# Kernel tuning notes

Hardware: AMD Instinct MI355X
Metric: run time of the kernel (lower is better)

The kernel has to match this reference:

```python
import jax, jax.numpy as jnp
import numpy as np

B = 512            # number of graphs in the batch
P = 256            # nodes per graph (== max_graph_size, graphs are equal-sized)
N = B * P          # total nodes
E = 2 * 1024 * 1024
F = 64             # node_feat_size
LAYERS = [32, 32, 32, 1]


def setup_inputs() -> dict:
    key = jax.random.key(0)
    ks = jax.random.split(key, 16)
    x = jax.random.normal(ks[0], (N, F), dtype=jnp.float32)
    edge_index = jax.random.randint(ks[1], (2, E), 0, N, dtype=jnp.int32)
    batch = (jnp.arange(N, dtype=jnp.int32) // P)   # sorted graph ids, equal sizes
    edge_mask = jax.random.uniform(ks[2], (E,), dtype=jnp.float32)
    # layer weights (DGCNN layer: out = D^-1 @ A_tilde @ X @ W + b)
    dims = [F] + LAYERS
    params = {}
    for i in range(len(LAYERS)):
        fan = dims[i]
        params[f"W{i}"] = jax.random.normal(ks[3 + 2 * i], (dims[i], dims[i + 1]), dtype=jnp.float32) / np.sqrt(fan)
        params[f"b{i}"] = jnp.zeros((dims[i + 1],), dtype=jnp.float32)
    return {"x": x, "edge_index": edge_index, "batch": batch, "edge_mask": edge_mask, **params}


def _build_matrices(x, edge_index, batch, edge_mask):
    # counts / exclusive starts per graph (batch is sorted)
    ones = jnp.ones_like(batch)
    counts = jax.ops.segment_sum(ones, batch, num_segments=B)
    starts = jnp.cumsum(counts) - counts                       # [B]
    src, dst = edge_index[0], edge_index[1]
    g = batch[src]
    valid = (batch[src] == batch[dst])                          # drop cross-graph edges
    ls = jnp.clip(src - starts[g], 0, P - 1)
    ld = jnp.clip(dst - starts[g], 0, P - 1)
    w = jnp.where(valid, edge_mask, 0.0)
    # padded A_tilde = A + I  (duplicate edges accumulate, as sparse COO add does)
    adj = jnp.zeros((B, P, P), dtype=x.dtype).at[g, ls, ld].add(w)
    adj = adj + jnp.eye(P, dtype=x.dtype)[None]
    # reciprocal degree of A_tilde, nan/inf -> 0
    deg = adj.sum(axis=2)                                       # [B, P]
    rinv = jnp.where(deg > 0, 1.0 / deg, 0.0)
    feats = x.reshape(B, P, F)                                  # equal-size graphs -> trivial pad
    return adj, rinv, feats


def reference(x, edge_index, batch, edge_mask, W0, b0, W1, b1, W2, b2, W3, b3):
    adj, rinv, h = _build_matrices(x, edge_index, batch, edge_mask)
    for W, b in ((W0, b0), (W1, b1), (W2, b2), (W3, b3)):
        h = jnp.einsum('bnm,bmf->bnf', adj, h @ W)              # A_tilde @ X @ W
        h = rinv[..., None] * h + b                             # D^-1 scaling + bias
        h = jnp.tanh(h)
    return h
```

## Files before the change

kernel.cpp:

```cpp
#include <hip/hip_runtime.h>
#include <hip/hip_bf16.h>

#define BGR 512
#define PP  256
#define NN  (BGR * PP)
#define EE  (2 * 1024 * 1024)
#define RCAP 4


__global__ void k_escatter(const int* __restrict__ ei, const float* __restrict__ emask,
                           int* __restrict__ rowcnt, int2* __restrict__ ebkt) {
    int e0 = (blockIdx.x * 256 + threadIdx.x) * 4;
    int4 s4 = *reinterpret_cast<const int4*>(ei + e0);
    int4 d4 = *reinterpret_cast<const int4*>(ei + EE + e0);
#pragma unroll
    for (int j = 0; j < 4; j++) {
        int s = (&s4.x)[j];
        int d = (&d4.x)[j];
        if ((s >> 8) != (d >> 8)) continue;
        float w = emask[e0 + j];
        int pos = atomicAdd(&rowcnt[s], 1);
        if (pos < RCAP) ebkt[s * RCAP + pos] = make_int2(d & 255, __float_as_int(w));
    }
}

__device__ __forceinline__ float fast_tanh(float x) {
    float t = __expf(2.0f * x);
    return 1.0f - __fdividef(2.0f, 1.0f + t);
}

template <int KH>
__device__ __forceinline__ void pmv32(const float (&h)[KH], const float* __restrict__ W,
                                      float (&P)[32]) {
#pragma unroll
    for (int c = 0; c < 32; c++) P[c] = 0.f;
#pragma unroll
    for (int k = 0; k < KH; k++) {
        const float hk = h[k];
#pragma unroll
        for (int c = 0; c < 32; c++) P[c] += hk * W[k * 32 + c];
    }
}

__global__ __launch_bounds__(512, 4)
void k_fused(const float* __restrict__ x,
             const float* __restrict__ W0, const float* __restrict__ b0,
             const float* __restrict__ W1, const float* __restrict__ b1,
             const float* __restrict__ W2, const float* __restrict__ b2,
             const float* __restrict__ W3, const float* __restrict__ b3,
             const int* __restrict__ rowcnt, const int2* __restrict__ ebkt,
             float* __restrict__ out) {
    __shared__ float Psl[2][PP][36];

    const int t    = threadIdx.x;
    const int g    = blockIdx.x;
    const int row  = t & 255;
    const int half = __builtin_amdgcn_readfirstlane(t >> 8);
    const int cb   = half * 16;

    const int node = g * PP + row;

    const int cnt = min(rowcnt[node], RCAP);
    int   eld[RCAP];
    float ewt[RCAP];
    float wsum = 0.f;
#pragma unroll
    for (int j = 0; j < RCAP; j++) {
        if (j < cnt) {
            int2 v = ebkt[node * RCAP + j];
            eld[j] = v.x;
            ewt[j] = __int_as_float(v.y);
            wsum += ewt[j];
        } else {
            eld[j] = row;
            ewt[j] = 0.f;
        }
    }
    const float rv = 1.0f / (1.0f + wsum);

    float xr[32];
    const float* xrow = x + (size_t)node * 64 + half * 32;
#pragma unroll
    for (int k = 0; k < 32; k += 4) {
        float4 v = *reinterpret_cast<const float4*>(xrow + k);
        xr[k] = v.x; xr[k + 1] = v.y; xr[k + 2] = v.z; xr[k + 3] = v.w;
    }

    float P[32];
    float acc[16];
    float h[16];

    const float* Ws0 = W0 + half * (32 * 32);
    const float* Ws1 = W1 + half * (16 * 32);
    const float* Ws2 = W2 + half * (16 * 32);

    float (*own)[36]       = Psl[half];
    const float (*par)[36] = Psl[1 - half];
    const float (*sA)[36]  = Psl[0];
    const float (*sB)[36]  = Psl[1];

#pragma unroll
    for (int L = 0; L < 3; L++) {
        if (L == 0)      pmv32<32>(xr, Ws0, P);
        else if (L == 1) pmv32<16>(h, Ws1, P);
        else             pmv32<16>(h, Ws2, P);

#pragma unroll
        for (int j = 0; j < 32; j += 4)
            *reinterpret_cast<float4*>(&own[row][j]) =
                make_float4(P[j], P[j + 1], P[j + 2], P[j + 3]);
        __syncthreads();

#pragma unroll
        for (int j = 0; j < 16; j += 4) {
            float4 q = *reinterpret_cast<const float4*>(&par[row][cb + j]);
            acc[j]     = P[cb + j]     + q.x;
            acc[j + 1] = P[cb + j + 1] + q.y;
            acc[j + 2] = P[cb + j + 2] + q.z;
            acc[j + 3] = P[cb + j + 3] + q.w;
        }

#pragma unroll
        for (int e = 0; e < RCAP; e++) {
            if (ewt[e] != 0.f) {
                int ld = eld[e];
                float w = ewt[e];
#pragma unroll
                for (int j = 0; j < 16; j += 4) {
                    float4 ya = *reinterpret_cast<const float4*>(&sA[ld][cb + j]);
                    float4 yb = *reinterpret_cast<const float4*>(&sB[ld][cb + j]);
                    acc[j]     += w * (ya.x + yb.x);
                    acc[j + 1] += w * (ya.y + yb.y);
                    acc[j + 2] += w * (ya.z + yb.z);
                    acc[j + 3] += w * (ya.w + yb.w);
                }
            }
        }

        const float* b = (L == 0) ? b0 : (L == 1) ? b1 : b2;
#pragma unroll
        for (int j = 0; j < 16; j++) h[j] = fast_tanh(rv * acc[j] + b[cb + j]);
        __syncthreads();
    }

    float a = 0.f;
#pragma unroll
    for (int k = 0; k < 16; k++) a += h[k] * W3[cb + k];
    Psl[0][row][32 + half] = a;
    __syncthreads();
    if (half == 0) {
        float z = Psl[0][row][32] + Psl[0][row][33];
#pragma unroll
        for (int e = 0; e < RCAP; e++) {
            if (ewt[e] != 0.f) {
                int ld = eld[e];
                z += ewt[e] * (Psl[0][ld][32] + Psl[0][ld][33]);
            }
        }
        out[node] = fast_tanh(rv * z + b3[0]);
    }
}


extern "C" void kernel_launch(void* const* d_in, const int* in_sizes, int n_in,
                              void* d_out, int out_size, void* d_ws, size_t ws_size,
                              hipStream_t stream) {
    const float* x     = (const float*)d_in[0];
    const int*   ei    = (const int*)d_in[1];
    const float* emask = (const float*)d_in[3];
    const float* W0 = (const float*)d_in[4];
    const float* b0 = (const float*)d_in[5];
    const float* W1 = (const float*)d_in[6];
    const float* b1 = (const float*)d_in[7];
    const float* W2 = (const float*)d_in[8];
    const float* b2 = (const float*)d_in[9];
    const float* W3 = (const float*)d_in[10];
    const float* b3 = (const float*)d_in[11];
    float* out = (float*)d_out;

    int*  rowcnt = (int*)d_ws;
    int2* ebkt   = (int2*)(rowcnt + NN);

    hipMemsetAsync(d_ws, 0, (size_t)NN * sizeof(int), stream);

    k_escatter<<<EE / 1024, 256, 0, stream>>>(ei, emask, rowcnt, ebkt);

    k_fused<<<BGR, 512, 0, stream>>>(x, W0, b0, W1, b1, W2, b2, W3, b3,
                                     rowcnt, ebkt, out);
}
```

Measured before the change: 130.7 us.

## Stage weights in LDS and exchange half-sums to cut neighbor gather reads

Copies W0, W1 and W2 into shared memory once per block and reads them with float4 loads instead of scalar global loads. The partial-product exchange changes: each half writes only the columns its partner needs, then stores the combined row sum back to a single shared buffer. The neighbor gather therefore reads one combined float4 per edge instead of two. The price is an extra barrier per layer plus a 16KB weight buffer in LDS, which together with the smaller partial buffer may change occupancy.

New measurement: 134.8 us. +3.2%, slower.

```diff
diff --git a/kernel.cpp b/kernel.cpp
--- a/kernel.cpp
+++ b/kernel.cpp
@@ -6,7 +6,6 @@
 #define NN  (BGR * PP)
 #define EE  (2 * 1024 * 1024)
 #define RCAP 4
-
 
 __global__ void k_escatter(const int* __restrict__ ei, const float* __restrict__ emask,
                            int* __restrict__ rowcnt, int2* __restrict__ ebkt) {
@@ -38,7 +37,13 @@
     for (int k = 0; k < KH; k++) {
         const float hk = h[k];
 #pragma unroll
-        for (int c = 0; c < 32; c++) P[c] += hk * W[k * 32 + c];
+        for (int c = 0; c < 32; c += 4) {
+            float4 w = *reinterpret_cast<const float4*>(W + k * 32 + c);
+            P[c]     += hk * w.x;
+            P[c + 1] += hk * w.y;
+            P[c + 2] += hk * w.z;
+            P[c + 3] += hk * w.w;
+        }
     }
 }
 
@@ -50,15 +55,23 @@
              const float* __restrict__ W3, const float* __restrict__ b3,
              const int* __restrict__ rowcnt, const int2* __restrict__ ebkt,
              float* __restrict__ out) {
-    __shared__ float Psl[2][PP][36];
+    __shared__ float Psl[PP][36];
+    __shared__ float Wl[4096];
 
     const int t    = threadIdx.x;
     const int g    = blockIdx.x;
     const int row  = t & 255;
     const int half = __builtin_amdgcn_readfirstlane(t >> 8);
     const int cb   = half * 16;
+    const int ob   = 16 - cb;
 
     const int node = g * PP + row;
+
+    reinterpret_cast<float4*>(Wl)[t] = reinterpret_cast<const float4*>(W0)[t];
+    if (half == 0)
+        reinterpret_cast<float4*>(Wl + 2048)[row] = reinterpret_cast<const float4*>(W1)[row];
+    else
+        reinterpret_cast<float4*>(Wl + 3072)[row] = reinterpret_cast<const float4*>(W2)[row];
 
     const int cnt = min(rowcnt[node], RCAP);
     int   eld[RCAP];
@@ -86,39 +99,41 @@
         xr[k] = v.x; xr[k + 1] = v.y; xr[k + 2] = v.z; xr[k + 3] = v.w;
     }
 
+    __syncthreads();
+
+    const float* Wp0 = Wl + half * 1024;
+    const float* Wp1 = Wl + 2048 + half * 512;
+    const float* Wp2 = Wl + 3072 + half * 512;
+
     float P[32];
     float acc[16];
     float h[16];
 
-    const float* Ws0 = W0 + half * (32 * 32);
-    const float* Ws1 = W1 + half * (16 * 32);
-    const float* Ws2 = W2 + half * (16 * 32);
-
-    float (*own)[36]       = Psl[half];
-    const float (*par)[36] = Psl[1 - half];
-    const float (*sA)[36]  = Psl[0];
-    const float (*sB)[36]  = Psl[1];
-
 #pragma unroll
     for (int L = 0; L < 3; L++) {
-        if (L == 0)      pmv32<32>(xr, Ws0, P);
-        else if (L == 1) pmv32<16>(h, Ws1, P);
-        else             pmv32<16>(h, Ws2, P);
-
-#pragma unroll
-        for (int j = 0; j < 32; j += 4)
-            *reinterpret_cast<float4*>(&own[row][j]) =
-                make_float4(P[j], P[j + 1], P[j + 2], P[j + 3]);
+        if (L == 0)      pmv32<32>(xr, Wp0, P);
+        else if (L == 1) pmv32<16>(h, Wp1, P);
+        else             pmv32<16>(h, Wp2, P);
+
+#pragma unroll
+        for (int j = 0; j < 16; j += 4)
+            *reinterpret_cast<float4*>(&Psl[row][ob + j]) =
+                make_float4(P[ob + j], P[ob + j + 1], P[ob + j + 2], P[ob + j + 3]);
         __syncthreads();
 
 #pragma unroll
         for (int j = 0; j < 16; j += 4) {
-            float4 q = *reinterpret_cast<const float4*>(&par[row][cb + j]);
+            float4 q = *reinterpret_cast<const float4*>(&Psl[row][cb + j]);
             acc[j]     = P[cb + j]     + q.x;
             acc[j + 1] = P[cb + j + 1] + q.y;
             acc[j + 2] = P[cb + j + 2] + q.z;
             acc[j + 3] = P[cb + j + 3] + q.w;
         }
+#pragma unroll
+        for (int j = 0; j < 16; j += 4)
+            *reinterpret_cast<float4*>(&Psl[row][cb + j]) =
+                make_float4(acc[j], acc[j + 1], acc[j + 2], acc[j + 3]);
+        __syncthreads();
 
 #pragma unroll
         for (int e = 0; e < RCAP; e++) {
@@ -127,12 +142,11 @@
                 float w = ewt[e];
 #pragma unroll
                 for (int j = 0; j < 16; j += 4) {
-                    float4 ya = *reinterpret_cast<const float4*>(&sA[ld][cb + j]);
-                    float4 yb = *reinterpret_cast<const float4*>(&sB[ld][cb + j]);
-                    acc[j]     += w * (ya.x + yb.x);
-                    acc[j + 1] += w * (ya.y + yb.y);
-                    acc[j + 2] += w * (ya.z + yb.z);
-                    acc[j + 3] += w * (ya.w + yb.w);
+                    float4 y = *reinterpret_cast<const float4*>(&Psl[ld][cb + j]);
+                    acc[j]     += w * y.x;
+                    acc[j + 1] += w * y.y;
+                    acc[j + 2] += w * y.z;
+                    acc[j + 3] += w * y.w;
                 }
             }
         }
@@ -146,15 +160,15 @@
     float a = 0.f;
 #pragma unroll
     for (int k = 0; k < 16; k++) a += h[k] * W3[cb + k];
-    Psl[0][row][32 + half] = a;
+    Psl[row][32 + half] = a;
     __syncthreads();
     if (half == 0) {
-        float z = Psl[0][row][32] + Psl[0][row][33];
+        float z = Psl[row][32] + Psl[row][33];
 #pragma unroll
         for (int e = 0; e < RCAP; e++) {
             if (ewt[e] != 0.f) {
                 int ld = eld[e];
-                z += ewt[e] * (Psl[0][ld][32] + Psl[0][ld][33]);
+                z += ewt[e] * (Psl[ld][32] + Psl[ld][33]);
             }
         }
         out[node] = fast_tanh(rv * z + b3[0]);
```
